# Performance work log

Hardware: AMD Instinct MI355X
Metric: run time of the kernel (lower is better)

## Reference

```python
import jax, jax.numpy as jnp
import numpy as np

N = 50000      # nodes
E = 1600000    # edges
F = 128        # num_feature
H = 256        # num_hidden
L = 3          # num_message_passing_steps
EPS = 1e-5     # LayerNorm eps (torch default)


def setup_inputs() -> dict:
    key = jax.random.key(0)
    ks = jax.random.split(key, 8)
    node = jax.random.normal(ks[0], (N, F), dtype=jnp.float32)
    edges = jax.random.randint(ks[1], (2, E), 0, N, dtype=jnp.int64)
    edges_attr = jax.random.uniform(ks[2], (E,), dtype=jnp.float32)
    sF = np.float32(1.0 / np.sqrt(F))
    sH = np.float32(1.0 / np.sqrt(H))
    W1 = jax.random.normal(ks[3], (F, H), dtype=jnp.float32) * sF
    b1 = jnp.zeros((H,), jnp.float32)
    W_convs = jax.random.normal(ks[4], (L, H, H), dtype=jnp.float32) * sH
    b_convs = jnp.zeros((L, H), jnp.float32)
    ln_g = jnp.ones((L, H), jnp.float32)
    ln_b = jnp.zeros((L, H), jnp.float32)
    fc_W = jax.random.normal(ks[5], (H, 2), dtype=jnp.float32) * sH
    fc_b = jnp.zeros((2,), jnp.float32)
    return dict(node=node, edges=edges, edges_attr=edges_attr, W1=W1, b1=b1,
                W_convs=W_convs, b_convs=b_convs, ln_g=ln_g, ln_b=ln_b,
                fc_W=fc_W, fc_b=fc_b)


def gcn_conv(x, src_a, dst_a, w_a, W, b):
    # PyG GCNConv: x' = D^-1/2 (A + I) D^-1/2 (x W) + b, edge weights w.
    # src_a/dst_a/w_a already include self-loops (weight 1).
    n = x.shape[0]
    xw = x @ W                                      # [N, H]
    deg = jax.ops.segment_sum(w_a, dst_a, num_segments=n)
    deg_safe = jnp.where(deg > 0, deg, 1.0)
    dinv = jnp.where(deg > 0, jax.lax.rsqrt(deg_safe), 0.0)
    norm = dinv[src_a] * w_a * dinv[dst_a]          # [E+N]
    msg = xw[src_a] * norm[:, None]                 # gather + scale
    out = jax.ops.segment_sum(msg, dst_a, num_segments=n)  # scatter-add
    return out + b


def layer_norm(x, g, b):
    mu = jnp.mean(x, axis=-1, keepdims=True)
    var = jnp.mean((x - mu) ** 2, axis=-1, keepdims=True)
    return (x - mu) * jax.lax.rsqrt(var + EPS) * g + b


def reference(node, edges, edges_attr, W1, b1, W_convs, b_convs, ln_g, ln_b, fc_W, fc_b):
    n = node.shape[0]
    loop = jnp.arange(n, dtype=edges.dtype)
    src_a = jnp.concatenate([edges[0], loop])
    dst_a = jnp.concatenate([edges[1], loop])
    w_a = jnp.concatenate([edges_attr, jnp.ones((n,), edges_attr.dtype)])

    x = gcn_conv(node, src_a, dst_a, w_a, W1, b1)
    for i in range(L):
        x_res = x
        x = gcn_conv(x, src_a, dst_a, w_a, W_convs[i], b_convs[i])
        x = layer_norm(x, ln_g[i], ln_b[i])
        x = jax.nn.relu(x + x_res)
    x = x @ fc_W + fc_b                              # [N, 2]
    return jnp.mean(x, axis=0, keepdims=True)        # global_mean_pool, batch=None -> [1, 2]
```

## Files before the change

### kernel.cpp

```cpp
#include <hip/hip_runtime.h>

#define EPS 1e-5f
#define WSCALE 65536.0f
#define NBK 64

typedef __attribute__((ext_vector_type(8))) short short8;
typedef __attribute__((ext_vector_type(4))) short short4v;
typedef __attribute__((ext_vector_type(4))) float float4v;
typedef __attribute__((ext_vector_type(2))) float float2v;
typedef __attribute__((ext_vector_type(8))) unsigned short ushort8;
typedef __attribute__((ext_vector_type(4))) unsigned int uint4v;

#if __has_builtin(__builtin_nontemporal_load)
#define NT_LOAD(p) __builtin_nontemporal_load(p)
#else
#define NT_LOAD(p) (*(p))
#endif

__device__ __forceinline__ unsigned short f2b(float f) {
    union { float f; unsigned u; } v; v.f = f;
    unsigned r = v.u + 0x7FFF + ((v.u >> 16) & 1);
    return (unsigned short)(r >> 16);
}
__device__ __forceinline__ float b2f(unsigned short u) {
    union { unsigned u; float f; } v; v.u = ((unsigned)u) << 16;
    return v.f;
}

__device__ __forceinline__ int qbucket(int cnt) {
    int qc = ((cnt + 4) & ~3) >> 2;
    return qc < NBK - 1 ? qc : NBK - 1;
}


__global__ __launch_bounds__(256) void rank_kernel(const int* __restrict__ dst,
                                                   const float* __restrict__ w,
                                                   unsigned int* __restrict__ combo,
                                                   int* __restrict__ rank, int E) {
    int e = blockIdx.x * 256 + threadIdx.x;
    if (e < E) {
        int d = dst[e];
        unsigned pack = (1u << 24) | (unsigned)(w[e] * WSCALE);
        unsigned old = atomicAdd(&combo[(size_t)d * 16], pack);
        rank[e] = (int)(old >> 24);
    }
}

__global__ __launch_bounds__(256) void dinv_hist_kernel(const unsigned int* __restrict__ combo,
                                                        float* __restrict__ dinv,
                                                        int* __restrict__ blockhist, int n) {
    __shared__ int lh[NBK];
    int t = threadIdx.x;
    if (t < NBK) lh[t] = 0;
    __syncthreads();
    int d = blockIdx.x * 256 + t;
    if (d < n) {
        unsigned cw = combo[(size_t)d * 16];
        int cnt = (int)(cw >> 24);
        float degv = (float)(cw & 0xffffffu) * (1.0f / WSCALE);
        dinv[d] = rsqrtf(degv + 1.0f);
        atomicAdd(&lh[qbucket(cnt)], 1);
    }
    __syncthreads();
    if (t < NBK) blockhist[blockIdx.x * NBK + t] = lh[t];
}

__global__ __launch_bounds__(256) void bin_prescan_kernel(const int* __restrict__ blockhist,
                                                          int* __restrict__ blockpre,
                                                          int* __restrict__ tot, int nblk) {
    int bkt = blockIdx.x;
    int t = threadIdx.x, lane = t & 63, w = t >> 6;
    __shared__ int wsum[4];
    __shared__ int s_carry;
    if (t == 0) s_carry = 0;
    __syncthreads();
    for (int base = 0; base < nblk; base += 256) {
        int i = base + t;
        int v = (i < nblk) ? blockhist[i * NBK + bkt] : 0;
        int x = v;
        for (int off = 1; off < 64; off <<= 1) {
            int u = __shfl_up(x, off);
            if (lane >= off) x += u;
        }
        if (lane == 63) wsum[w] = x;
        __syncthreads();
        if (t == 0) {
            int a = wsum[0];
            wsum[0] = 0;
            for (int k = 1; k < 4; ++k) { int b = wsum[k]; wsum[k] = a; a += b; }
            wsum[0] = 0;
        }
        __syncthreads();
        int carry = s_carry;
        int woff = wsum[w];
        if (i < nblk) blockpre[i * NBK + bkt] = carry + woff + x - v;
        __syncthreads();
        if (t == 255) s_carry = carry + woff + x;
        __syncthreads();
    }
    if (t == 0) tot[bkt] = s_carry;
}

__global__ __launch_bounds__(64) void bin_suffix_kernel(const int* __restrict__ tot,
                                                        int* __restrict__ base) {
    int t = threadIdx.x;
    int v = tot[t];
    int s = v;
    for (int off = 1; off < 64; off <<= 1) {
        int u = __shfl_down(s, off);
        if (t + off < 64) s += u;
    }
    base[t] = s - v;
}

__global__ __launch_bounds__(256) void bin_scatter_kernel(const unsigned int* __restrict__ combo,
                                                          const int* __restrict__ base,
                                                          const int* __restrict__ blockpre,
                                                          int* __restrict__ perm,
                                                          int* __restrict__ posod,
                                                          int* __restrict__ qlen, int n) {
    __shared__ int lcur[NBK];
    int t = threadIdx.x;
    if (t < NBK) lcur[t] = base[t] + blockpre[blockIdx.x * NBK + t];
    __syncthreads();
    int d = blockIdx.x * 256 + t;
    if (d < n) {
        int cnt = (int)(combo[(size_t)d * 16] >> 24);
        int pos = atomicAdd(&lcur[qbucket(cnt)], 1);
        perm[pos] = d;
        posod[d] = pos;
        qlen[pos] = (cnt + 4) & ~3;
    }
}


__global__ __launch_bounds__(1024) void scan_local_kernel(const int* __restrict__ qlen,
                                                          int* __restrict__ row_ptr,
                                                          int* __restrict__ bsum, int n) {
    int tid = threadIdx.x, lane = tid & 63, w = tid >> 6;
    __shared__ int wsum[16];
    int i = blockIdx.x * 1024 + tid;
    int v = (i < n) ? qlen[i] : 0;
    int x = v;
    for (int off = 1; off < 64; off <<= 1) {
        int t = __shfl_up(x, off);
        if (lane >= off) x += t;
    }
    if (lane == 63) wsum[w] = x;
    __syncthreads();
    if (w == 0 && lane < 16) {
        int s = wsum[lane];
        for (int off = 1; off < 16; off <<= 1) {
            int t = __shfl_up(s, off, 16);
            if (lane >= off) s += t;
        }
        wsum[lane] = s;
    }
    __syncthreads();
    int woff = (w > 0) ? wsum[w - 1] : 0;
    if (i < n) row_ptr[i + 1] = woff + x;
    if (tid == 0) bsum[blockIdx.x] = wsum[15];
}

__global__ __launch_bounds__(64) void scan_mid_kernel(int* __restrict__ bsum,
                                                      int* __restrict__ row_ptr, int nb) {
    int t = threadIdx.x;
    int carry = 0;
    for (int base = 0; base < nb; base += 64) {
        int idx = base + t;
        int v = (idx < nb) ? bsum[idx] : 0;
        int x = v;
        for (int off = 1; off < 64; off <<= 1) {
            int u = __shfl_up(x, off);
            if (t >= off) x += u;
        }
        if (idx < nb) bsum[idx] = carry + x - v;
        carry += __shfl(x, 63);
    }
    if (t == 0) row_ptr[0] = 0;
}

__global__ __launch_bounds__(1024) void scan_add_kernel(const int* __restrict__ bsum,
                                                        int* __restrict__ row_ptr, int n) {
    int i = blockIdx.x * 1024 + threadIdx.x;
    if (i < n) row_ptr[i + 1] += bsum[blockIdx.x];
}

__global__ __launch_bounds__(256) void selfpad_kernel(const unsigned int* __restrict__ combo,
                                                      const int* __restrict__ row_ptr,
                                                      const int* __restrict__ posod,
                                                      const float* __restrict__ dinv,
                                                      unsigned int* __restrict__ edge, int n) {
    int d = blockIdx.x * 256 + threadIdx.x;
    if (d < n) {
        int cnt = (int)(combo[(size_t)d * 16] >> 24);
        int slot = posod[d];
        int j0 = row_ptr[slot], j1 = row_ptr[slot + 1];
        float di = dinv[d];
        edge[j0] = ((unsigned)f2b(di * di) << 16) | (unsigned)slot;
        for (int j = j0 + 1 + cnt; j < j1; ++j) edge[j] = (unsigned)slot;
    }
}

__global__ __launch_bounds__(256) void scatter2_kernel(
    const int* __restrict__ src, const int* __restrict__ dst,
    const float* __restrict__ w, const int* __restrict__ rank,
    const int* __restrict__ row_ptr, const int* __restrict__ posod,
    const float* __restrict__ dinv, unsigned int* __restrict__ edge, int E) {
    int e = blockIdx.x * 256 + threadIdx.x;
    if (e < E) {
        int d = dst[e], s = src[e];
        float wn = dinv[s] * w[e] * dinv[d];
        edge[row_ptr[posod[d]] + 1 + rank[e]] = ((unsigned)f2b(wn) << 16) | (unsigned)posod[s];
    }
}

__global__ __launch_bounds__(256) void cast_sliced_kernel(const float* __restrict__ in,
                                                          const int* __restrict__ perm,
                                                          unsigned short* __restrict__ out,
                                                          int n, int F) {
    int idx = blockIdx.x * 256 + threadIdx.x;
    if (idx < n * (F / 4)) {
        int f4 = idx * 4;
        int slot = f4 / F, f = f4 - slot * F;
        float4 v = *(const float4*)&in[(size_t)perm[slot] * F + f];
        short4v s = (short4v){(short)f2b(v.x), (short)f2b(v.y), (short)f2b(v.z), (short)f2b(v.w)};
        *(short4v*)&out[((size_t)(f >> 5) * n + slot) * 32 + (f & 31)] = s;
    }
}

__global__ __launch_bounds__(256) void wtransL_kernel(const float* __restrict__ W,
                                                      unsigned short* __restrict__ Wt,
                                                      int K, int Nc, int total) {
    int o = blockIdx.x * 256 + threadIdx.x;
    if (o < total) {
        int l = o / (K * Nc);
        int r = o - l * K * Nc;
        int n = r / K, k = r - n * K;
        Wt[o] = f2b(W[(size_t)l * K * Nc + (size_t)k * Nc + n]);
    }
}


#define GST 88

template <bool SLICEOUT>
__global__ __launch_bounds__(256) void gemm_n256(const unsigned short* __restrict__ A,
                                                 const unsigned short* __restrict__ Bt,
                                                 unsigned short* __restrict__ Cout,
                                                 const float* __restrict__ bias,
                                                 int M, int K) {
    __shared__ __align__(16) short As[64 * GST];
    __shared__ __align__(16) short Bs[256 * GST];
    int t = threadIdx.x;
    int lane = t & 63, w = t >> 6;
    int quad = lane >> 4, l16 = lane & 15;
    int row0 = blockIdx.x * 64;

    float4v acc[16];
#pragma unroll
    for (int c = 0; c < 16; ++c) acc[c] = (float4v){0.f, 0.f, 0.f, 0.f};

    int arow = t >> 2, ak16 = (t & 3) * 16;
    int bcol0 = t >> 2, bko = (t & 3) * 16;

    for (int k_outer = 0; k_outer < K; k_outer += 64) {
        bool rowok = (row0 + arow) < M;
        const unsigned short* ap = &A[(size_t)(row0 + arow) * K + k_outer + ak16];
        uint4 z = make_uint4(0, 0, 0, 0);
        uint4 u0 = rowok ? *(const uint4*)ap : z;
        uint4 u1 = rowok ? *(const uint4*)(ap + 8) : z;
        *(uint4*)&As[arow * GST + ak16] = u0;
        *(uint4*)&As[arow * GST + ak16 + 8] = u1;
#pragma unroll
        for (int cb = 0; cb < 4; ++cb) {
            int col = bcol0 + 64 * cb;
            const unsigned short* bp = &Bt[(size_t)col * K + k_outer + bko];
#pragma unroll
            for (int u = 0; u < 2; ++u)
                *(uint4*)&Bs[col * GST + bko + u * 8] = *(const uint4*)&bp[u * 8];
        }
        __syncthreads();
#pragma unroll
        for (int k0 = 0; k0 < 64; k0 += 32) {
            short8 a = *(const short8*)&As[(w * 16 + l16) * GST + k0 + quad * 8];
#pragma unroll
            for (int c = 0; c < 16; ++c) {
                short8 b = *(const short8*)&Bs[(c * 16 + l16) * GST + k0 + quad * 8];
                acc[c] = __builtin_amdgcn_mfma_f32_16x16x32_bf16(a, b, acc[c], 0, 0, 0);
            }
        }
        __syncthreads();
    }
#pragma unroll
    for (int c = 0; c < 16; ++c) {
        int col = c * 16 + l16;
        float bcol = (!SLICEOUT) ? bias[col] : 0.0f;
#pragma unroll
        for (int r = 0; r < 4; ++r) {
            int row = row0 + w * 16 + quad * 4 + r;
            if (row < M) {
                if (SLICEOUT)
                    Cout[((size_t)(c >> 1) * M + row) * 32 + ((c & 1) << 4) + l16] = f2b(acc[c][r]);
                else
                    Cout[(size_t)row * 256 + col] = f2b(acc[c][r] + bcol);
            }
        }
    }
}


#define CAPQ 1024

template <int CSH>
__global__ __launch_bounds__(256) void agg_grp(
    const unsigned short* __restrict__ tab0, const int* __restrict__ row_ptr,
    const unsigned int* __restrict__ edge, unsigned short* __restrict__ outb, int n) {
    __shared__ uint4v eq[CAPQ];
    int b = blockIdx.x;
    int s = b & ((1 << CSH) - 1);
    int grp = b >> CSH;
    int t = threadIdx.x;
    int d0 = grp * 64;
    int d = d0 + (t >> 2);

    const uint4v* e4p = (const uint4v*)edge;
    int qbase = row_ptr[d0] >> 2;
    int dmax = d0 + 64 < n ? d0 + 64 : n;
    int qcnt = (row_ptr[dmax] >> 2) - qbase;
    int qstage = qcnt < CAPQ ? qcnt : CAPQ;
    for (int i = t; i < qstage; i += 256) eq[i] = NT_LOAD(&e4p[qbase + i]);
    __syncthreads();

    if (d >= n) return;
    int fo = (t & 3) << 3;
    const unsigned short* tab = tab0 + (size_t)s * n * 32;

    int j = row_ptr[d] >> 2, j1 = row_ptr[d + 1] >> 2;
    int jmid = j1 < qbase + CAPQ ? j1 : qbase + CAPQ;

    float2v a2[4];
#pragma unroll
    for (int k = 0; k < 4; ++k) a2[k] = (float2v){0.f, 0.f};

    auto process = [&](uint4v e4) {
#pragma unroll
        for (int u = 0; u < 4; ++u) {
            unsigned e = e4[u];
            float wq = __int_as_float((int)(e & 0xffff0000u));
            float2v w2 = {wq, wq};
            unsigned off = ((e & 0xffffu) << 5) + (unsigned)fo;
            uint4 rr = *(const uint4*)(tab + off);
            unsigned uu0 = rr.x, uu1 = rr.y, uu2 = rr.z, uu3 = rr.w;
            float2v f0 = {__uint_as_float(uu0 << 16), __uint_as_float(uu0 & 0xffff0000u)};
            float2v f1 = {__uint_as_float(uu1 << 16), __uint_as_float(uu1 & 0xffff0000u)};
            float2v f2 = {__uint_as_float(uu2 << 16), __uint_as_float(uu2 & 0xffff0000u)};
            float2v f3 = {__uint_as_float(uu3 << 16), __uint_as_float(uu3 & 0xffff0000u)};
            a2[0] += f0 * w2;
            a2[1] += f1 * w2;
            a2[2] += f2 * w2;
            a2[3] += f3 * w2;
        }
    };

    for (; j + 2 <= jmid; j += 2) {
        uint4v e4a = eq[j - qbase];
        uint4v e4b = eq[j + 1 - qbase];
        process(e4a);
        process(e4b);
    }
    if (j < jmid) { process(eq[j - qbase]); ++j; }
    for (; j < j1; ++j) process(NT_LOAD(&e4p[j]));

    ushort8 o;
#pragma unroll
    for (int k = 0; k < 4; ++k) {
        o[2 * k] = f2b(a2[k].x);
        o[2 * k + 1] = f2b(a2[k].y);
    }
    *(ushort8*)(outb + ((size_t)d << (5 + CSH)) + (s << 5) + fo) = o;
}


__global__ __launch_bounds__(256) void ln_res_relu(
    const unsigned short* __restrict__ preln, const float* __restrict__ bias,
    const float* __restrict__ g, const float* __restrict__ lb,
    const unsigned short* __restrict__ res, unsigned short* __restrict__ out, int n) {
    int wv = __builtin_amdgcn_readfirstlane(threadIdx.x >> 6);
    int d = blockIdx.x * 4 + wv;
    if (d >= n) return;
    int l = threadIdx.x & 63;
    int fo = l * 4;
    ushort4 pv = *(const ushort4*)&preln[(size_t)d * 256 + fo];
    float4 bb = *(const float4*)&bias[fo];
    float v[4] = {b2f(pv.x) + bb.x, b2f(pv.y) + bb.y, b2f(pv.z) + bb.z, b2f(pv.w) + bb.w};
    float s4 = v[0] + v[1] + v[2] + v[3];
#pragma unroll
    for (int off = 1; off < 64; off <<= 1) s4 += __shfl_xor(s4, off);
    float mu = s4 * (1.0f / 256.0f);
    float dv[4];
    float qs = 0.f;
#pragma unroll
    for (int j = 0; j < 4; ++j) { dv[j] = v[j] - mu; qs += dv[j] * dv[j]; }
#pragma unroll
    for (int off = 1; off < 64; off <<= 1) qs += __shfl_xor(qs, off);
    float rs = rsqrtf(qs * (1.0f / 256.0f) + EPS);

    float4 gg = *(const float4*)&g[fo];
    float4 lbv = *(const float4*)&lb[fo];
    ushort4 rr4 = *(const ushort4*)&res[(size_t)d * 256 + fo];
    float ggv[4] = {gg.x, gg.y, gg.z, gg.w};
    float lbvv[4] = {lbv.x, lbv.y, lbv.z, lbv.w};
    float rrv[4] = {b2f(rr4.x), b2f(rr4.y), b2f(rr4.z), b2f(rr4.w)};
    ushort4 o;
    unsigned short* op = (unsigned short*)&o;
#pragma unroll
    for (int j = 0; j < 4; ++j) {
        float x = dv[j] * rs * ggv[j] + lbvv[j] + rrv[j];
        op[j] = f2b(x > 0.f ? x : 0.f);
    }
    *(ushort4*)&out[(size_t)d * 256 + fo] = o;
}


__global__ __launch_bounds__(256) void colsum_kernel(const unsigned short* __restrict__ x,
                                                     float* __restrict__ sums, int n) {
    int h = threadIdx.x;
    float acc = 0.0f;
    for (int r = blockIdx.x; r < n; r += gridDim.x) acc += b2f(x[(size_t)r * 256 + h]);
    atomicAdd(&sums[h], acc);
}

__global__ __launch_bounds__(64) void final_kernel(const float* __restrict__ sums,
                                                   const float* __restrict__ fcW,
                                                   const float* __restrict__ fcb,
                                                   float* __restrict__ out, float invN) {
    int lane = threadIdx.x;
    float p0 = 0.0f, p1 = 0.0f;
    for (int hh = lane; hh < 256; hh += 64) {
        float m = sums[hh];
        p0 += m * fcW[hh * 2 + 0];
        p1 += m * fcW[hh * 2 + 1];
    }
    for (int off = 32; off > 0; off >>= 1) {
        p0 += __shfl_down(p0, off);
        p1 += __shfl_down(p1, off);
    }
    if (lane == 0) {
        out[0] = p0 * invN + fcb[0];
        out[1] = p1 * invN + fcb[1];
    }
}


extern "C" void kernel_launch(void* const* d_in, const int* in_sizes, int n_in,
                              void* d_out, int out_size, void* d_ws, size_t ws_size,
                              hipStream_t stream) {
    const float* node    = (const float*)d_in[0];
    const int*   edges   = (const int*)d_in[1];
    const float* eattr   = (const float*)d_in[2];
    const float* W1      = (const float*)d_in[3];
    const float* b1      = (const float*)d_in[4];
    const float* W_convs = (const float*)d_in[5];
    const float* b_convs = (const float*)d_in[6];
    const float* ln_g    = (const float*)d_in[7];
    const float* ln_b    = (const float*)d_in[8];
    const float* fc_W    = (const float*)d_in[9];
    const float* fc_b    = (const float*)d_in[10];
    float* out = (float*)d_out;

    const int H = in_sizes[4];
    const int F = in_sizes[3] / H;
    const int N = in_sizes[0] / F;
    const int E = in_sizes[2];
    const int L = in_sizes[6] / H;

    const int* src = edges;
    const int* dst = edges + E;

    char* p = (char*)d_ws;
    auto alloc = [&](size_t bytes) {
        char* r = p;
        p += (bytes + 255) & ~(size_t)255;
        return r;
    };
    int nblk = (N + 255) / 256;
    int nb1024 = (N + 1023) / 1024;
    unsigned int* combo = (unsigned int*)alloc((size_t)N * 64);
    float* colsums = (float*)alloc((size_t)H * 4);
    size_t zero_bytes = (size_t)((char*)colsums - (char*)combo) + (((size_t)H * 4 + 255) & ~(size_t)255);
    int*   blockhist = (int*)alloc((size_t)nblk * NBK * 4);
    int*   blockpre  = (int*)alloc((size_t)nblk * NBK * 4);
    int*   tot       = (int*)alloc((size_t)NBK * 4);
    int*   bbase     = (int*)alloc((size_t)NBK * 4);
    int*   perm    = (int*)alloc((size_t)N * 4);
    int*   posod   = (int*)alloc((size_t)N * 4);
    int*   qlen    = (int*)alloc((size_t)N * 4);
    float* dinv    = (float*)alloc((size_t)N * 4);
    int*   row_ptr = (int*)alloc((size_t)(N + 1) * 4);
    int*   bsum    = (int*)alloc((size_t)nb1024 * 4);
    unsigned int* edge = (unsigned int*)alloc(((size_t)E + 4 * (size_t)N + 64) * 4);
    unsigned short* Wt1 = (unsigned short*)alloc((size_t)H * F * 2);
    unsigned short* Wtc = (unsigned short*)alloc((size_t)L * H * H * 2);
    unsigned short* xw  = (unsigned short*)alloc((size_t)N * H * 2);
    unsigned short* preln = (unsigned short*)alloc((size_t)N * H * 2);
    unsigned short* bufA  = (unsigned short*)alloc((size_t)N * H * 2);
    unsigned short* bufB  = (unsigned short*)alloc((size_t)N * H * 2);
    int*            rank  = (int*)xw;
    unsigned short* nodeb = preln;
    unsigned short* aggn  = preln + (size_t)N * F;

    hipMemsetAsync(combo, 0, zero_bytes, stream);

    int gE = (E + 255) / 256;
    rank_kernel<<<gE, 256, 0, stream>>>(dst, eattr, combo, rank, E);
    dinv_hist_kernel<<<nblk, 256, 0, stream>>>(combo, dinv, blockhist, N);
    bin_prescan_kernel<<<NBK, 256, 0, stream>>>(blockhist, blockpre, tot, nblk);
    bin_suffix_kernel<<<1, 64, 0, stream>>>(tot, bbase);
    bin_scatter_kernel<<<nblk, 256, 0, stream>>>(combo, bbase, blockpre, perm, posod, qlen, N);
    scan_local_kernel<<<nb1024, 1024, 0, stream>>>(qlen, row_ptr, bsum, N);
    scan_mid_kernel<<<1, 64, 0, stream>>>(bsum, row_ptr, nb1024);
    scan_add_kernel<<<nb1024, 1024, 0, stream>>>(bsum, row_ptr, N);
    selfpad_kernel<<<nblk, 256, 0, stream>>>(combo, row_ptr, posod, dinv, edge, N);
    scatter2_kernel<<<gE, 256, 0, stream>>>(src, dst, eattr, rank, row_ptr, posod, dinv, edge, E);

    cast_sliced_kernel<<<(N * (F / 4) + 255) / 256, 256, 0, stream>>>(node, perm, nodeb, N, F);
    wtransL_kernel<<<(F * H + 255) / 256, 256, 0, stream>>>(W1, Wt1, F, H, F * H);
    wtransL_kernel<<<(L * H * H + 255) / 256, 256, 0, stream>>>(W_convs, Wtc, H, H, L * H * H);

    int ngrp64 = (N + 63) / 64;
    int lngrid = (N + 3) / 4;
    int ggrid = (N + 63) / 64;

    agg_grp<2><<<4 * ngrp64, 256, 0, stream>>>(nodeb, row_ptr, edge, aggn, N);
    gemm_n256<false><<<ggrid, 256, 0, stream>>>(aggn, Wt1, bufA, b1, N, F);

    unsigned short* x = bufA;
    unsigned short* other = bufB;
    for (int i = 0; i < L; ++i) {
        gemm_n256<true><<<ggrid, 256, 0, stream>>>(x, Wtc + (size_t)i * H * H, xw, nullptr, N, H);
        agg_grp<3><<<8 * ngrp64, 256, 0, stream>>>(xw, row_ptr, edge, preln, N);
        ln_res_relu<<<lngrid, 256, 0, stream>>>(preln, b_convs + (size_t)i * H,
                                                ln_g + (size_t)i * H, ln_b + (size_t)i * H,
                                                x, other, N);
        unsigned short* t = x; x = other; other = t;
    }

    colsum_kernel<<<256, 256, 0, stream>>>(x, colsums, N);
    final_kernel<<<1, 64, 0, stream>>>(colsums, fc_W, fc_b, out, 1.0f / (float)N);
}
```

Before: 683.0 us.

## Store gathered feature tables in FP8 to halve aggregation gather traffic

Converts the gathered node-feature tables (input features and per-layer x@W outputs) from bf16 to FP8 E4M3 with 64-byte slices, and changes the aggregation kernel to decode FP8 pairs with hardware conversion. Each thread now handles 16 features per edge, and there are half as many feature slices. This targets the memory bandwidth of the random gathers in message passing, which dominate runtime. The cost is precision: FP8 has a 3-bit mantissa and no scaling, which may break tolerance. The GEMM epilogue also gains cross-lane shuffles to pack FP8 bytes.

```diff
diff --git a/kernel.cpp b/kernel.cpp
--- a/kernel.cpp
+++ b/kernel.cpp
@@ -215,17 +215,18 @@
     }
 }
 
-__global__ __launch_bounds__(256) void cast_sliced_kernel(const float* __restrict__ in,
-                                                          const int* __restrict__ perm,
-                                                          unsigned short* __restrict__ out,
-                                                          int n, int F) {
+__global__ __launch_bounds__(256) void cast_sliced_fp8(const float* __restrict__ in,
+                                                       const int* __restrict__ perm,
+                                                       unsigned char* __restrict__ out,
+                                                       int n, int F) {
     int idx = blockIdx.x * 256 + threadIdx.x;
     if (idx < n * (F / 4)) {
         int f4 = idx * 4;
         int slot = f4 / F, f = f4 - slot * F;
         float4 v = *(const float4*)&in[(size_t)perm[slot] * F + f];
-        short4v s = (short4v){(short)f2b(v.x), (short)f2b(v.y), (short)f2b(v.z), (short)f2b(v.w)};
-        *(short4v*)&out[((size_t)(f >> 5) * n + slot) * 32 + (f & 31)] = s;
+        int p = __builtin_amdgcn_cvt_pk_fp8_f32(v.x, v.y, 0, false);
+        p = __builtin_amdgcn_cvt_pk_fp8_f32(v.z, v.w, p, true);
+        *(unsigned int*)&out[((size_t)(f >> 6) * n + slot) * 64 + (f & 63)] = (unsigned)p;
     }
 }
 
@@ -292,18 +293,37 @@
         }
         __syncthreads();
     }
-#pragma unroll
-    for (int c = 0; c < 16; ++c) {
-        int col = c * 16 + l16;
-        float bcol = (!SLICEOUT) ? bias[col] : 0.0f;
-#pragma unroll
-        for (int r = 0; r < 4; ++r) {
-            int row = row0 + w * 16 + quad * 4 + r;
-            if (row < M) {
-                if (SLICEOUT)
-                    Cout[((size_t)(c >> 1) * M + row) * 32 + ((c & 1) << 4) + l16] = f2b(acc[c][r]);
-                else
-                    Cout[(size_t)row * 256 + col] = f2b(acc[c][r] + bcol);
+    if (SLICEOUT) {
+        unsigned char* c8 = (unsigned char*)Cout;
+#pragma unroll
+        for (int c = 0; c < 16; ++c) {
+#pragma unroll
+            for (int r = 0; r < 4; ++r) {
+                float v = acc[c][r];
+                float vn = __shfl_xor(v, 1);
+                int pair = __builtin_amdgcn_cvt_pk_fp8_f32(v, vn, 0, false);
+                int p2 = __shfl_xor(pair, 2);
+                int quad32 = (pair & 0xffff) | (p2 << 16);
+                int b4 = __shfl_xor(quad32, 4);
+                int b8 = __shfl_xor(quad32, 8);
+                int b12 = __shfl_xor(b4, 8);
+                int row = row0 + w * 16 + quad * 4 + r;
+                if (l16 == 0 && row < M) {
+                    uint4 ov = make_uint4((unsigned)quad32, (unsigned)b4,
+                                          (unsigned)b8, (unsigned)b12);
+                    *(uint4*)&c8[((size_t)(c >> 2) * M + row) * 64 + ((c & 3) << 4)] = ov;
+                }
+            }
+        }
+    } else {
+#pragma unroll
+        for (int c = 0; c < 16; ++c) {
+            int col = c * 16 + l16;
+            float bcol = bias[col];
+#pragma unroll
+            for (int r = 0; r < 4; ++r) {
+                int row = row0 + w * 16 + quad * 4 + r;
+                if (row < M) Cout[(size_t)row * 256 + col] = f2b(acc[c][r] + bcol);
             }
         }
     }
@@ -314,7 +334,7 @@
 
 template <int CSH>
 __global__ __launch_bounds__(256) void agg_grp(
-    const unsigned short* __restrict__ tab0, const int* __restrict__ row_ptr,
+    const unsigned char* __restrict__ tab0, const int* __restrict__ row_ptr,
     const unsigned int* __restrict__ edge, unsigned short* __restrict__ outb, int n) {
     __shared__ uint4v eq[CAPQ];
     int b = blockIdx.x;
@@ -333,15 +353,15 @@
     __syncthreads();
 
     if (d >= n) return;
-    int fo = (t & 3) << 3;
-    const unsigned short* tab = tab0 + (size_t)s * n * 32;
+    int fo = (t & 3) << 4;
+    const unsigned char* tab = tab0 + (size_t)s * n * 64;
 
     int j = row_ptr[d] >> 2, j1 = row_ptr[d + 1] >> 2;
     int jmid = j1 < qbase + CAPQ ? j1 : qbase + CAPQ;
 
-    float2v a2[4];
-#pragma unroll
-    for (int k = 0; k < 4; ++k) a2[k] = (float2v){0.f, 0.f};
+    float2v a2[8];
+#pragma unroll
+    for (int k = 0; k < 8; ++k) a2[k] = (float2v){0.f, 0.f};
 
     auto process = [&](uint4v e4) {
 #pragma unroll
@@ -349,17 +369,16 @@
             unsigned e = e4[u];
             float wq = __int_as_float((int)(e & 0xffff0000u));
             float2v w2 = {wq, wq};
-            unsigned off = ((e & 0xffffu) << 5) + (unsigned)fo;
+            unsigned off = ((e & 0xffffu) << 6) + (unsigned)fo;
             uint4 rr = *(const uint4*)(tab + off);
-            unsigned uu0 = rr.x, uu1 = rr.y, uu2 = rr.z, uu3 = rr.w;
-            float2v f0 = {__uint_as_float(uu0 << 16), __uint_as_float(uu0 & 0xffff0000u)};
-            float2v f1 = {__uint_as_float(uu1 << 16), __uint_as_float(uu1 & 0xffff0000u)};
-            float2v f2 = {__uint_as_float(uu2 << 16), __uint_as_float(uu2 & 0xffff0000u)};
-            float2v f3 = {__uint_as_float(uu3 << 16), __uint_as_float(uu3 & 0xffff0000u)};
-            a2[0] += f0 * w2;
-            a2[1] += f1 * w2;
-            a2[2] += f2 * w2;
-            a2[3] += f3 * w2;
+#pragma unroll
+            for (int k = 0; k < 4; ++k) {
+                unsigned uu = (&rr.x)[k];
+                float2v lo = __builtin_amdgcn_cvt_pk_f32_fp8(uu, false);
+                float2v hi = __builtin_amdgcn_cvt_pk_f32_fp8(uu, true);
+                a2[2 * k] += lo * w2;
+                a2[2 * k + 1] += hi * w2;
+            }
         }
     };
 
@@ -372,13 +391,17 @@
     if (j < jmid) { process(eq[j - qbase]); ++j; }
     for (; j < j1; ++j) process(NT_LOAD(&e4p[j]));
 
-    ushort8 o;
+    ushort8 o0, o1;
 #pragma unroll
     for (int k = 0; k < 4; ++k) {
-        o[2 * k] = f2b(a2[k].x);
-        o[2 * k + 1] = f2b(a2[k].y);
-    }
-    *(ushort8*)(outb + ((size_t)d << (5 + CSH)) + (s << 5) + fo) = o;
+        o0[2 * k] = f2b(a2[k].x);
+        o0[2 * k + 1] = f2b(a2[k].y);
+        o1[2 * k] = f2b(a2[4 + k].x);
+        o1[2 * k + 1] = f2b(a2[4 + k].y);
+    }
+    size_t obase = ((size_t)d << (6 + CSH)) + (s << 6) + fo;
+    *(ushort8*)(outb + obase) = o0;
+    *(ushort8*)(outb + obase + 8) = o1;
 }
 
 
@@ -502,12 +525,12 @@
     unsigned int* edge = (unsigned int*)alloc(((size_t)E + 4 * (size_t)N + 64) * 4);
     unsigned short* Wt1 = (unsigned short*)alloc((size_t)H * F * 2);
     unsigned short* Wtc = (unsigned short*)alloc((size_t)L * H * H * 2);
-    unsigned short* xw  = (unsigned short*)alloc((size_t)N * H * 2);
+    unsigned char*  xw  = (unsigned char*)alloc((size_t)N * H);
     unsigned short* preln = (unsigned short*)alloc((size_t)N * H * 2);
     unsigned short* bufA  = (unsigned short*)alloc((size_t)N * H * 2);
     unsigned short* bufB  = (unsigned short*)alloc((size_t)N * H * 2);
     int*            rank  = (int*)xw;
-    unsigned short* nodeb = preln;
+    unsigned char*  nodeb = (unsigned char*)preln;
     unsigned short* aggn  = preln + (size_t)N * F;
 
     hipMemsetAsync(combo, 0, zero_bytes, stream);
@@ -524,7 +547,7 @@
     selfpad_kernel<<<nblk, 256, 0, stream>>>(combo, row_ptr, posod, dinv, edge, N);
     scatter2_kernel<<<gE, 256, 0, stream>>>(src, dst, eattr, rank, row_ptr, posod, dinv, edge, E);
 
-    cast_sliced_kernel<<<(N * (F / 4) + 255) / 256, 256, 0, stream>>>(node, perm, nodeb, N, F);
+    cast_sliced_fp8<<<(N * (F / 4) + 255) / 256, 256, 0, stream>>>(node, perm, nodeb, N, F);
     wtransL_kernel<<<(F * H + 255) / 256, 256, 0, stream>>>(W1, Wt1, F, H, F * H);
     wtransL_kernel<<<(L * H * H + 255) / 256, 256, 0, stream>>>(W_convs, Wtc, H, H, L * H * H);
 
@@ -532,14 +555,15 @@
     int lngrid = (N + 3) / 4;
     int ggrid = (N + 63) / 64;
 
-    agg_grp<2><<<4 * ngrp64, 256, 0, stream>>>(nodeb, row_ptr, edge, aggn, N);
+    agg_grp<1><<<2 * ngrp64, 256, 0, stream>>>(nodeb, row_ptr, edge, aggn, N);
     gemm_n256<false><<<ggrid, 256, 0, stream>>>(aggn, Wt1, bufA, b1, N, F);
 
     unsigned short* x = bufA;
     unsigned short* other = bufB;
     for (int i = 0; i < L; ++i) {
-        gemm_n256<true><<<ggrid, 256, 0, stream>>>(x, Wtc + (size_t)i * H * H, xw, nullptr, N, H);
-        agg_grp<3><<<8 * ngrp64, 256, 0, stream>>>(xw, row_ptr, edge, preln, N);
+        gemm_n256<true><<<ggrid, 256, 0, stream>>>(x, Wtc + (size_t)i * H * H,
+                                                   (unsigned short*)xw, nullptr, N, H);
+        agg_grp<2><<<4 * ngrp64, 256, 0, stream>>>(xw, row_ptr, edge, preln, N);
         ln_res_relu<<<lngrid, 256, 0, stream>>>(preln, b_convs + (size_t)i * H,
                                                 ln_g + (size_t)i * H, ln_b + (size_t)i * H,
                                                 x, other, N);
```

Result: faster. 630.3 us, median of 2 (-7.7%).
